# Kernel optimization log

Hardware: AMD Instinct MI355X
Metric: run time of the kernel (lower is better)

## Reference

```python
import jax, jax.numpy as jnp
import numpy as np

N = 50000   # nodes
E = 500000  # edges (before self-loops)
H = 4       # heads
C = 128     # per-head channels
DIN = 182
D1 = H * C  # 512
LN_EPS = 1e-5
NEG_SLOPE = 0.2


def setup_inputs():
    key = jax.random.key(0)
    ks = jax.random.split(key, 26)
    def rn(k, shape, s=0.05):
        return jax.random.normal(k, shape, jnp.float32) * s
    return {
        'x': jax.random.normal(ks[0], (N, DIN), jnp.float32),
        'edge_index': jax.random.randint(ks[1], (2, E), 0, N, jnp.int32),
        # GAT layer 1 (182 -> 4x128)
        'W1': rn(ks[2], (DIN, D1)), 'as1': rn(ks[3], (H, C)), 'ad1': rn(ks[4], (H, C)), 'b1': rn(ks[5], (D1,)),
        # LayerNorm 1
        'g1': jnp.ones((D1,), jnp.float32), 'bn1': jnp.zeros((D1,), jnp.float32),
        # Expansion MLP 512->512->256
        'We1': rn(ks[6], (D1, D1)), 'bE1': rn(ks[7], (D1,)),
        'We2': rn(ks[8], (D1, 256)), 'bE2': rn(ks[9], (256,)),
        # Residual projection 512->256 + learned scale
        'Wr': rn(ks[10], (D1, 256)), 'br': rn(ks[11], (256,)),
        'rscale': jnp.float32(0.5),
        # GAT layer 2 (256 -> 4x128)
        'W2': rn(ks[12], (256, D1)), 'as2': rn(ks[13], (H, C)), 'ad2': rn(ks[14], (H, C)), 'b2': rn(ks[15], (D1,)),
        # LayerNorm 2
        'g2': jnp.ones((D1,), jnp.float32), 'bn2': jnp.zeros((D1,), jnp.float32),
        # Classifier 512->512->2
        'Wc1': rn(ks[16], (D1, D1)), 'bc1': rn(ks[17], (D1,)),
        'Wc2': rn(ks[18], (D1, 2)), 'bc2': rn(ks[19], (2,)),
    }


def layer_norm(x, g, b):
    mu = jnp.mean(x, axis=-1, keepdims=True)
    var = jnp.mean(jnp.square(x - mu), axis=-1, keepdims=True)
    return (x - mu) * jax.lax.rsqrt(var + LN_EPS) * g + b


def gat_conv(x, src, dst, W, a_src, a_dst, bias):
    # PyG GATConv (eval mode, self-loops already in src/dst), concat heads.
    h = (x @ W).reshape(N, H, C)                     # [N,H,C]
    al_s = jnp.sum(h * a_src, axis=-1)               # [N,H]
    al_d = jnp.sum(h * a_dst, axis=-1)               # [N,H]
    e = jax.nn.leaky_relu(al_s[src] + al_d[dst], NEG_SLOPE)  # [E',H]
    m = jax.ops.segment_max(e, dst, num_segments=N)  # segment softmax over target nbhd
    ex = jnp.exp(e - m[dst])
    denom = jax.ops.segment_sum(ex, dst, num_segments=N)
    alpha = ex / denom[dst]                          # [E',H]
    msg = h[src] * alpha[:, :, None]                 # [E',H,C]
    out = jax.ops.segment_sum(msg, dst, num_segments=N)
    return out.reshape(N, H * C) + bias


def reference(x, edge_index, W1, as1, ad1, b1, g1, bn1, We1, bE1, We2, bE2,
              Wr, br, rscale, W2, as2, ad2, b2, g2, bn2, Wc1, bc1, Wc2, bc2):
    loops = jnp.arange(N, dtype=edge_index.dtype)
    src = jnp.concatenate([edge_index[0], loops])    # add self-loops (PyG default)
    dst = jnp.concatenate([edge_index[1], loops])

    h1 = gat_conv(x, src, dst, W1, as1, ad1, b1)
    h1 = jax.nn.elu(layer_norm(h1, g1, bn1))
    h_exp = jax.nn.relu(h1 @ We1 + bE1) @ We2 + bE2  # expansion MLP (dropout=eval)
    h_comb = (h1 @ Wr + br) + rscale * h_exp         # residual combine

    h2 = gat_conv(h_comb, src, dst, W2, as2, ad2, b2)
    h2 = jax.nn.elu(layer_norm(h2, g2, bn2))
    out = jax.nn.relu(h2 @ Wc1 + bc1) @ Wc2 + bc2    # classifier -> [N,2]
    return out
```

## Files before the change

kernel.cpp:

```cpp
#include <hip/hip_runtime.h>
#include <hip/hip_bf16.h>
#include <math.h>

#define NNODES 50000
#define NEDGES 500000
#define NTOT   (NEDGES + NNODES)
#define MPAD   50048
#define D1     512
#define NH     4
#define LN_EPS 1e-5f
#define NEG_SLOPE 0.2f

#define SBLK 256
#define NSB  ((NNODES + SBLK - 1) / SBLK)

typedef __attribute__((ext_vector_type(8))) short short8;
typedef __attribute__((ext_vector_type(4))) float f32x4;
typedef __hip_bfloat16 bf16;

#define GLDS16(g, l) __builtin_amdgcn_global_load_lds( \
    (const __attribute__((address_space(1))) void*)(g), \
    (__attribute__((address_space(3))) void*)(l), 16, 0, 0)

__device__ __forceinline__ float bf2f(short u) {
    unsigned int x = ((unsigned int)(unsigned short)u) << 16;
    return __uint_as_float(x);
}
__device__ __forceinline__ short f2bf(float f) {
    unsigned int x = __float_as_uint(f);
    unsigned int r = (x + 0x7fffu + ((x >> 16) & 1u)) >> 16;
    return (short)r;
}
__device__ __forceinline__ float leaky(float e) {
    return (e >= 0.f) ? e : NEG_SLOPE * e;
}


__global__ void k_count(const int* __restrict__ ei, int* __restrict__ counts) {
    int e = blockIdx.x * blockDim.x + threadIdx.x;
    if (e >= NTOT) return;
    int d = (e < NEDGES) ? ei[NEDGES + e] : (e - NEDGES);
    atomicAdd(&counts[d], 1);
}

__global__ void k_scan1(const int* __restrict__ counts, int* __restrict__ offs,
                        int* __restrict__ bsums) {
    __shared__ int s[SBLK];
    int tid = threadIdx.x, b = blockIdx.x;
    int idx = b * SBLK + tid;
    int v = (idx < NNODES) ? counts[idx] : 0;
    s[tid] = v;
    __syncthreads();
    for (int d = 1; d < SBLK; d <<= 1) {
        int t = (tid >= d) ? s[tid - d] : 0;
        __syncthreads();
        s[tid] += t;
        __syncthreads();
    }
    if (idx < NNODES) offs[idx] = s[tid] - v;
    if (tid == SBLK - 1) bsums[b] = s[tid];
}

__global__ void k_scan2(const int* __restrict__ bsums, int* __restrict__ bbase) {
    __shared__ int s[256];
    int tid = threadIdx.x;
    int v = (tid < NSB) ? bsums[tid] : 0;
    s[tid] = v;
    __syncthreads();
    for (int d = 1; d < 256; d <<= 1) {
        int t = (tid >= d) ? s[tid - d] : 0;
        __syncthreads();
        s[tid] += t;
        __syncthreads();
    }
    bbase[tid] = s[tid] - v;
    if (tid == 255) bbase[256] = s[255];
}

__global__ void k_scan3(int* __restrict__ offs, const int* __restrict__ bbase,
                        int* __restrict__ cursor) {
    int idx = blockIdx.x * 256 + threadIdx.x;
    if (idx < NNODES) {
        int v = offs[idx] + bbase[idx >> 8];
        offs[idx] = v;
        cursor[idx] = v;
    }
    if (idx == 0) offs[NNODES] = bbase[256];
}

__global__ void k_fill(const int* __restrict__ ei, int* __restrict__ cursor,
                       int* __restrict__ srcs) {
    int e = blockIdx.x * blockDim.x + threadIdx.x;
    if (e >= NTOT) return;
    int s, d;
    if (e < NEDGES) { s = ei[e]; d = ei[NEDGES + e]; }
    else            { s = d = e - NEDGES; }
    int pos = atomicAdd(&cursor[d], 1);
    srcs[pos] = s;
}


__global__ void k_wt_all(const float* __restrict__ W1, const float* __restrict__ We1,
                         const float* __restrict__ We2, const float* __restrict__ Wr,
                         const float* __restrict__ W2, const float* __restrict__ Wc1,
                         bf16* __restrict__ W1t, bf16* __restrict__ We1t,
                         bf16* __restrict__ We2t, bf16* __restrict__ Wrt,
                         bf16* __restrict__ W2t, bf16* __restrict__ Wc1t) {
    int which = blockIdx.y;
    const float* W; bf16* Wt; int K, N, Kpad;
    switch (which) {
        case 0:  W = W1;  Wt = W1t;  K = 182; N = 512; Kpad = 192; break;
        case 1:  W = We1; Wt = We1t; K = 512; N = 512; Kpad = 512; break;
        case 2:  W = We2; Wt = We2t; K = 512; N = 256; Kpad = 512; break;
        case 3:  W = Wr;  Wt = Wrt;  K = 512; N = 256; Kpad = 512; break;
        case 4:  W = W2;  Wt = W2t;  K = 256; N = 512; Kpad = 256; break;
        default: W = Wc1; Wt = Wc1t; K = 512; N = 512; Kpad = 512; break;
    }
    int idx = blockIdx.x * 256 + threadIdx.x;
    if (idx >= N * Kpad) return;
    int n = idx / Kpad, k = idx % Kpad;
    float v = (k < K) ? W[(size_t)k * N + n] : 0.f;
    Wt[idx] = __float2bfloat16(v);
}

__global__ void k_xconv(const float* __restrict__ x, bf16* __restrict__ xb) {
    int idx = blockIdx.x * 256 + threadIdx.x;
    if (idx >= MPAD * 192) return;
    int r = idx / 192, k = idx % 192;
    float v = (r < NNODES && k < 182) ? x[(size_t)r * 182 + k] : 0.f;
    xb[idx] = __float2bfloat16(v);
}


__global__ __launch_bounds__(256) void k_attn_logits(
        const bf16* __restrict__ h, const float* __restrict__ a_s,
        const float* __restrict__ a_d, float* __restrict__ als,
        float* __restrict__ ald) {
    int tid = threadIdx.x;
    int n = blockIdx.x * 4 + (tid >> 6);
    if (n >= NNODES) return;
    int lane = tid & 63;
    int ch0 = lane * 8;
    short8 hv = *reinterpret_cast<const short8*>(&h[(size_t)n * D1 + ch0]);
    float s1 = 0.f, s2 = 0.f;
    #pragma unroll
    for (int j = 0; j < 8; j++) {
        float v = bf2f(hv[j]);
        s1 += v * a_s[ch0 + j];
        s2 += v * a_d[ch0 + j];
    }
    #pragma unroll
    for (int o = 1; o < 16; o <<= 1) {
        s1 += __shfl_xor(s1, o);
        s2 += __shfl_xor(s2, o);
    }
    if ((lane & 15) == 0) {
        int head = lane >> 4;
        als[n * NH + head] = s1;
        ald[n * NH + head] = s2;
    }
}


__global__ __launch_bounds__(256) void k_edge_alpha(
        const float* __restrict__ als, const float* __restrict__ ald,
        const int* __restrict__ offs, const int* __restrict__ srcs,
        float* __restrict__ alpha) {
    int tid = threadIdx.x;
    int n = blockIdx.x * 4 + (tid >> 6);
    if (n >= NNODES) return;
    int lane = tid & 63;
    int head = lane >> 4, sub = lane & 15;
    int e0 = offs[n], e1 = offs[n + 1];
    float adh = ald[n * NH + head];

    float m = -1e30f;
    for (int k = e0 + sub; k < e1; k += 16)
        m = fmaxf(m, leaky(als[srcs[k] * NH + head] + adh));
    #pragma unroll
    for (int o = 1; o < 16; o <<= 1) m = fmaxf(m, __shfl_xor(m, o));
    float d = 0.f;
    for (int k = e0 + sub; k < e1; k += 16)
        d += __expf(leaky(als[srcs[k] * NH + head] + adh) - m);
    #pragma unroll
    for (int o = 1; o < 16; o <<= 1) d += __shfl_xor(d, o);
    float dinv = 1.f / d;
    for (int k = e0 + sub; k < e1; k += 16)
        alpha[k * NH + head] = __expf(leaky(als[srcs[k] * NH + head] + adh) - m) * dinv;
}


__global__ __launch_bounds__(256) void k_gat_aggregate(
        const bf16* __restrict__ h, const float* __restrict__ alpha,
        const int* __restrict__ offs, const int* __restrict__ srcs,
        const float* __restrict__ bias, const float* __restrict__ gamma,
        const float* __restrict__ beta, bf16* __restrict__ out) {
    int tid = threadIdx.x;
    int n = blockIdx.x * 4 + (tid >> 6);
    if (n >= NNODES) return;
    int lane = tid & 63;
    int head = lane >> 4;
    int ch0 = lane * 8;
    int e0 = offs[n], e1 = offs[n + 1];

    float acc[8] = {};
    for (int base = e0; base < e1; base += 64) {
        int cnt = min(64, e1 - base);
        int sv = (base + lane < e1) ? srcs[base + lane] : 0;
        int k = 0;
        for (; k + 4 <= cnt; k += 4) {
            int s0 = __shfl(sv, k),     s1 = __shfl(sv, k + 1);
            int s2 = __shfl(sv, k + 2), s3 = __shfl(sv, k + 3);
            float p0 = alpha[(base + k)     * NH + head];
            float p1 = alpha[(base + k + 1) * NH + head];
            float p2 = alpha[(base + k + 2) * NH + head];
            float p3 = alpha[(base + k + 3) * NH + head];
            short8 h0 = *reinterpret_cast<const short8*>(&h[(size_t)s0 * D1 + ch0]);
            short8 h1 = *reinterpret_cast<const short8*>(&h[(size_t)s1 * D1 + ch0]);
            short8 h2 = *reinterpret_cast<const short8*>(&h[(size_t)s2 * D1 + ch0]);
            short8 h3 = *reinterpret_cast<const short8*>(&h[(size_t)s3 * D1 + ch0]);
            #pragma unroll
            for (int j = 0; j < 8; j++)
                acc[j] += p0 * bf2f(h0[j]) + p1 * bf2f(h1[j])
                        + p2 * bf2f(h2[j]) + p3 * bf2f(h3[j]);
        }
        for (; k < cnt; k++) {
            int s0 = __shfl(sv, k);
            float p0 = alpha[(base + k) * NH + head];
            short8 h0 = *reinterpret_cast<const short8*>(&h[(size_t)s0 * D1 + ch0]);
            #pragma unroll
            for (int j = 0; j < 8; j++) acc[j] += p0 * bf2f(h0[j]);
        }
    }

    float v[8];
    float ps = 0.f;
    #pragma unroll
    for (int j = 0; j < 8; j++) { v[j] = acc[j] + bias[ch0 + j]; ps += v[j]; }
    #pragma unroll
    for (int o = 1; o < 64; o <<= 1) ps += __shfl_xor(ps, o);
    float mu = ps * (1.f / 512.f);
    float qs = 0.f;
    #pragma unroll
    for (int j = 0; j < 8; j++) { float dvj = v[j] - mu; qs += dvj * dvj; }
    #pragma unroll
    for (int o = 1; o < 64; o <<= 1) qs += __shfl_xor(qs, o);
    float rstd = rsqrtf(qs * (1.f / 512.f) + LN_EPS);

    short8 ov;
    #pragma unroll
    for (int j = 0; j < 8; j++) {
        float y = (v[j] - mu) * rstd * gamma[ch0 + j] + beta[ch0 + j];
        float e = (y > 0.f) ? y : (__expf(y) - 1.f);
        ov[j] = f2bf(e);
    }
    *reinterpret_cast<short8*>(&out[(size_t)n * D1 + ch0]) = ov;
}


#define EPI_BF       0
#define EPI_BRELU_BF 1
#define EPI_CLS      2

template<int EPI>
__global__ __launch_bounds__(256) void gemm_bf16(
    const ushort* __restrict__ A, const ushort* __restrict__ Bt,
    const float* __restrict__ bias, bf16* __restrict__ Obf,
    float* __restrict__ Of32, const float* __restrict__ Wc2,
    int Mreal, int N, int K, const float* __restrict__ bc2) {
    __shared__ __align__(16) ushort As[128 * 32];
    __shared__ __align__(16) ushort Bs[128 * 32];
    int tid = threadIdx.x;
    int wave = tid >> 6, lane = tid & 63;
    int brow = blockIdx.y * 128;
    int bcol = blockIdx.x * 128;
    int wm = (wave >> 1) * 64, wn = (wave & 1) * 64;

    f32x4 acc[4][4] = {};

    int ldr = lane >> 2;
    int ldk = (lane & 3) * 8;

    for (int k0 = 0; k0 < K; k0 += 32) {
        if (k0) __syncthreads();
        #pragma unroll
        for (int c2 = 0; c2 < 2; c2++) {
            int c = wave + c2 * 4;
            int row = c * 16 + ldr;
            GLDS16(A  + (size_t)(brow + row) * K + k0 + ldk, As + c * 512);
            GLDS16(Bt + (size_t)(bcol + row) * K + k0 + ldk, Bs + c * 512);
        }
        __syncthreads();

        short8 af[4], bfr[4];
        int lr = lane & 15, lk = (lane >> 4) * 8;
        #pragma unroll
        for (int f = 0; f < 4; f++) {
            af[f]  = *reinterpret_cast<const short8*>(&As[(wm + f * 16 + lr) * 32 + lk]);
            bfr[f] = *reinterpret_cast<const short8*>(&Bs[(wn + f * 16 + lr) * 32 + lk]);
        }
        #pragma unroll
        for (int fm = 0; fm < 4; fm++)
            #pragma unroll
            for (int fn = 0; fn < 4; fn++)
                acc[fm][fn] = __builtin_amdgcn_mfma_f32_16x16x32_bf16(
                    af[fm], bfr[fn], acc[fm][fn], 0, 0, 0);
    }

    if (EPI == EPI_CLS) {
        float w2[4][2], b4[4];
        #pragma unroll
        for (int fn = 0; fn < 4; fn++) {
            int col = bcol + wn + fn * 16 + (lane & 15);
            w2[fn][0] = Wc2[col * 2];
            w2[fn][1] = Wc2[col * 2 + 1];
            b4[fn] = bias[col];
        }
        #pragma unroll
        for (int fm = 0; fm < 4; fm++) {
            #pragma unroll
            for (int r = 0; r < 4; r++) {
                int row = brow + wm + fm * 16 + (lane >> 4) * 4 + r;
                float s0 = 0.f, s1 = 0.f;
                #pragma unroll
                for (int fn = 0; fn < 4; fn++) {
                    float v = acc[fm][fn][r] + b4[fn];
                    v = v > 0.f ? v : 0.f;
                    s0 += v * w2[fn][0];
                    s1 += v * w2[fn][1];
                }
                #pragma unroll
                for (int o = 1; o < 16; o <<= 1) {
                    s0 += __shfl_xor(s0, o);
                    s1 += __shfl_xor(s1, o);
                }
                if ((lane & 15) == 0 && row < Mreal) {
                    if (bcol == 0 && wn == 0) { s0 += bc2[0]; s1 += bc2[1]; }
                    atomicAdd(&Of32[row * 2],     s0);
                    atomicAdd(&Of32[row * 2 + 1], s1);
                }
            }
        }
        return;
    }

    #pragma unroll
    for (int fm = 0; fm < 4; fm++) {
        int row0 = brow + wm + fm * 16 + (lane >> 4) * 4;
        #pragma unroll
        for (int fn = 0; fn < 4; fn++) {
            int col = bcol + wn + fn * 16 + (lane & 15);
            #pragma unroll
            for (int r = 0; r < 4; r++) {
                int row = row0 + r;
                if (row >= Mreal) continue;
                size_t idx = (size_t)row * N + col;
                float v = acc[fm][fn][r];
                if (EPI == EPI_BF) {
                    Obf[idx] = __float2bfloat16(v);
                } else {
                    v += bias[col]; v = v > 0.f ? v : 0.f;
                    Obf[idx] = __float2bfloat16(v);
                }
            }
        }
    }
}


__global__ __launch_bounds__(256) void gemm_dual(
    const ushort* __restrict__ A1, const ushort* __restrict__ B1t,
    const ushort* __restrict__ A2, const ushort* __restrict__ B2t,
    const float* __restrict__ bias1, const float* __restrict__ bias2,
    bf16* __restrict__ Obf, int Mreal, int N, int K,
    const float* __restrict__ rsc) {
    __shared__ __align__(16) ushort As[128 * 32];
    __shared__ __align__(16) ushort Bs[128 * 32];
    int tid = threadIdx.x;
    int wave = tid >> 6, lane = tid & 63;
    int brow = blockIdx.y * 128;
    int bcol = blockIdx.x * 128;
    int wm = (wave >> 1) * 64, wn = (wave & 1) * 64;
    float rs = *rsc;

    f32x4 acc[4][4] = {};

    int ldr = lane >> 2;
    int ldk = (lane & 3) * 8;
    int lr = lane & 15, lk = (lane >> 4) * 8;

    #pragma unroll
    for (int phase = 0; phase < 2; phase++) {
        const ushort* Ap = phase ? A2 : A1;
        const ushort* Bp = phase ? B2t : B1t;
        if (phase) {
            __syncthreads();
            #pragma unroll
            for (int fm = 0; fm < 4; fm++)
                #pragma unroll
                for (int fn = 0; fn < 4; fn++)
                    #pragma unroll
                    for (int r = 0; r < 4; r++) acc[fm][fn][r] *= rs;
        }
        for (int k0 = 0; k0 < K; k0 += 32) {
            if (k0 || phase) __syncthreads();
            #pragma unroll
            for (int c2 = 0; c2 < 2; c2++) {
                int c = wave + c2 * 4;
                int row = c * 16 + ldr;
                GLDS16(Ap + (size_t)(brow + row) * K + k0 + ldk, As + c * 512);
                GLDS16(Bp + (size_t)(bcol + row) * K + k0 + ldk, Bs + c * 512);
            }
            __syncthreads();

            short8 af[4], bfr[4];
            #pragma unroll
            for (int f = 0; f < 4; f++) {
                af[f]  = *reinterpret_cast<const short8*>(&As[(wm + f * 16 + lr) * 32 + lk]);
                bfr[f] = *reinterpret_cast<const short8*>(&Bs[(wn + f * 16 + lr) * 32 + lk]);
            }
            #pragma unroll
            for (int fm = 0; fm < 4; fm++)
                #pragma unroll
                for (int fn = 0; fn < 4; fn++)
                    acc[fm][fn] = __builtin_amdgcn_mfma_f32_16x16x32_bf16(
                        af[fm], bfr[fn], acc[fm][fn], 0, 0, 0);
        }
    }

    #pragma unroll
    for (int fm = 0; fm < 4; fm++) {
        int row0 = brow + wm + fm * 16 + (lane >> 4) * 4;
        #pragma unroll
        for (int fn = 0; fn < 4; fn++) {
            int col = bcol + wn + fn * 16 + (lane & 15);
            float be = bias2[col] + rs * bias1[col];
            #pragma unroll
            for (int r = 0; r < 4; r++) {
                int row = row0 + r;
                if (row >= Mreal) continue;
                Obf[(size_t)row * N + col] = __float2bfloat16(acc[fm][fn][r] + be);
            }
        }
    }
}


extern "C" void kernel_launch(void* const* d_in, const int* in_sizes, int n_in,
                              void* d_out, int out_size, void* d_ws, size_t ws_size,
                              hipStream_t stream) {
    const float* x   = (const float*)d_in[0];
    const int*   ei  = (const int*)d_in[1];
    const float* W1  = (const float*)d_in[2];
    const float* as1 = (const float*)d_in[3];
    const float* ad1 = (const float*)d_in[4];
    const float* b1  = (const float*)d_in[5];
    const float* g1  = (const float*)d_in[6];
    const float* bn1 = (const float*)d_in[7];
    const float* We1 = (const float*)d_in[8];
    const float* bE1 = (const float*)d_in[9];
    const float* We2 = (const float*)d_in[10];
    const float* bE2 = (const float*)d_in[11];
    const float* Wr  = (const float*)d_in[12];
    const float* br  = (const float*)d_in[13];
    const float* rsc = (const float*)d_in[14];
    const float* W2  = (const float*)d_in[15];
    const float* as2 = (const float*)d_in[16];
    const float* ad2 = (const float*)d_in[17];
    const float* b2  = (const float*)d_in[18];
    const float* g2  = (const float*)d_in[19];
    const float* bn2 = (const float*)d_in[20];
    const float* Wc1 = (const float*)d_in[21];
    const float* bc1 = (const float*)d_in[22];
    const float* Wc2 = (const float*)d_in[23];
    const float* bc2 = (const float*)d_in[24];
    float* out = (float*)d_out;

    char* ws = (char*)d_ws;
    size_t o = 0;
    auto alloc = [&](size_t bytes) { void* p = ws + o; o += (bytes + 255) & ~255ull; return p; };
    bf16* xb    = (bf16*)alloc((size_t)MPAD * 192 * 2);
    bf16* bufA  = (bf16*)alloc((size_t)MPAD * D1 * 2);
    bf16* bufB  = (bf16*)alloc((size_t)MPAD * D1 * 2);
    bf16* bufC  = (bf16*)alloc((size_t)MPAD * D1 * 2);
    bf16* hcb   = (bf16*)alloc((size_t)MPAD * 256 * 2);
    bf16* W1t   = (bf16*)alloc((size_t)512 * 192 * 2);
    bf16* We1t  = (bf16*)alloc((size_t)512 * 512 * 2);
    bf16* We2t  = (bf16*)alloc((size_t)256 * 512 * 2);
    bf16* Wrt   = (bf16*)alloc((size_t)256 * 512 * 2);
    bf16* W2t   = (bf16*)alloc((size_t)512 * 256 * 2);
    bf16* Wc1t  = (bf16*)alloc((size_t)512 * 512 * 2);
    float* als  = (float*)alloc((size_t)NNODES * NH * 4);
    float* ald  = (float*)alloc((size_t)NNODES * NH * 4);
    float* alpha= (float*)alloc((size_t)NTOT * NH * 4);
    int* counts = (int*)alloc((NNODES + 1) * 4);
    int* offs   = (int*)alloc((NNODES + 1) * 4);
    int* cursor = (int*)alloc((NNODES + 1) * 4);
    int* srcs   = (int*)alloc((size_t)NTOT * 4);
    int* bsums  = (int*)alloc((NSB + 1) * 4);
    int* bbase  = (int*)alloc(257 * 4);

    hipMemsetAsync(counts, 0, NNODES * 4, stream);
    k_count<<<(NTOT + 255) / 256, 256, 0, stream>>>(ei, counts);
    k_scan1<<<NSB, SBLK, 0, stream>>>(counts, offs, bsums);
    k_scan2<<<1, 256, 0, stream>>>(bsums, bbase);
    k_scan3<<<(NNODES + 255) / 256, 256, 0, stream>>>(offs, bbase, cursor);
    k_fill<<<(NTOT + 255) / 256, 256, 0, stream>>>(ei, cursor, srcs);

    k_wt_all<<<dim3(1024, 6), 256, 0, stream>>>(W1, We1, We2, Wr, W2, Wc1,
                                                W1t, We1t, We2t, Wrt, W2t, Wc1t);
    k_xconv<<<(MPAD * 192 + 255) / 256, 256, 0, stream>>>(x, xb);

    dim3 blk(256);
    dim3 g512(4, MPAD / 128), g256(2, MPAD / 128);
    int nwb = (NNODES + 3) / 4;

    gemm_bf16<EPI_BF><<<g512, blk, 0, stream>>>((const ushort*)xb, (const ushort*)W1t,
        nullptr, bufA, nullptr, nullptr, NNODES, 512, 192, nullptr);
    k_attn_logits<<<nwb, blk, 0, stream>>>(bufA, as1, ad1, als, ald);
    k_edge_alpha<<<nwb, blk, 0, stream>>>(als, ald, offs, srcs, alpha);
    k_gat_aggregate<<<nwb, blk, 0, stream>>>(bufA, alpha, offs, srcs, b1, g1, bn1, bufB);

    gemm_bf16<EPI_BRELU_BF><<<g512, blk, 0, stream>>>((const ushort*)bufB, (const ushort*)We1t,
        bE1, bufC, nullptr, nullptr, NNODES, 512, 512, nullptr);
    gemm_dual<<<g256, blk, 0, stream>>>((const ushort*)bufC, (const ushort*)We2t,
        (const ushort*)bufB, (const ushort*)Wrt, bE2, br, hcb, NNODES, 256, 512, rsc);

    gemm_bf16<EPI_BF><<<g512, blk, 0, stream>>>((const ushort*)hcb, (const ushort*)W2t,
        nullptr, bufA, nullptr, nullptr, NNODES, 512, 256, nullptr);
    k_attn_logits<<<nwb, blk, 0, stream>>>(bufA, as2, ad2, als, ald);
    k_edge_alpha<<<nwb, blk, 0, stream>>>(als, ald, offs, srcs, alpha);
    k_gat_aggregate<<<nwb, blk, 0, stream>>>(bufA, alpha, offs, srcs, b2, g2, bn2, bufB);

    hipMemsetAsync(out, 0, (size_t)out_size * 4, stream);
    gemm_bf16<EPI_CLS><<<g512, blk, 0, stream>>>((const ushort*)bufB, (const ushort*)Wc1t,
        bc1, nullptr, out, Wc2, NNODES, 512, 512, bc2);
}
```

Measured before the change: 561.0 us.

## Use K=64 swizzled LDS tiles, fuse attention logits into GEMM epilogue, reorder grid

```diff
diff --git a/kernel.cpp b/kernel.cpp
--- a/kernel.cpp
+++ b/kernel.cpp
@@ -129,36 +129,6 @@
     int r = idx / 192, k = idx % 192;
     float v = (r < NNODES && k < 182) ? x[(size_t)r * 182 + k] : 0.f;
     xb[idx] = __float2bfloat16(v);
-}
-
-
-__global__ __launch_bounds__(256) void k_attn_logits(
-        const bf16* __restrict__ h, const float* __restrict__ a_s,
-        const float* __restrict__ a_d, float* __restrict__ als,
-        float* __restrict__ ald) {
-    int tid = threadIdx.x;
-    int n = blockIdx.x * 4 + (tid >> 6);
-    if (n >= NNODES) return;
-    int lane = tid & 63;
-    int ch0 = lane * 8;
-    short8 hv = *reinterpret_cast<const short8*>(&h[(size_t)n * D1 + ch0]);
-    float s1 = 0.f, s2 = 0.f;
-    #pragma unroll
-    for (int j = 0; j < 8; j++) {
-        float v = bf2f(hv[j]);
-        s1 += v * a_s[ch0 + j];
-        s2 += v * a_d[ch0 + j];
-    }
-    #pragma unroll
-    for (int o = 1; o < 16; o <<= 1) {
-        s1 += __shfl_xor(s1, o);
-        s2 += __shfl_xor(s2, o);
-    }
-    if ((lane & 15) == 0) {
-        int head = lane >> 4;
-        als[n * NH + head] = s1;
-        ald[n * NH + head] = s2;
-    }
 }
 
 
@@ -258,60 +228,102 @@
 }
 
 
-#define EPI_BF       0
+#define EPI_BF_LOG   0
 #define EPI_BRELU_BF 1
 #define EPI_CLS      2
 
 template<int EPI>
-__global__ __launch_bounds__(256) void gemm_bf16(
+__global__ __launch_bounds__(256) void gemm64(
     const ushort* __restrict__ A, const ushort* __restrict__ Bt,
     const float* __restrict__ bias, bf16* __restrict__ Obf,
     float* __restrict__ Of32, const float* __restrict__ Wc2,
-    int Mreal, int N, int K, const float* __restrict__ bc2) {
-    __shared__ __align__(16) ushort As[128 * 32];
-    __shared__ __align__(16) ushort Bs[128 * 32];
+    int Mreal, int N, int K, const float* __restrict__ bc2,
+    const float* __restrict__ a_s, const float* __restrict__ a_d,
+    float* __restrict__ als, float* __restrict__ ald) {
+    __shared__ __align__(16) ushort As[128 * 64];
+    __shared__ __align__(16) ushort Bs[128 * 64];
     int tid = threadIdx.x;
     int wave = tid >> 6, lane = tid & 63;
-    int brow = blockIdx.y * 128;
-    int bcol = blockIdx.x * 128;
+    int brow = blockIdx.x * 128;
+    int bcol = blockIdx.y * 128;
     int wm = (wave >> 1) * 64, wn = (wave & 1) * 64;
+    int lr = lane & 15, hi = lane >> 4;
+    int rx = lr & 7;
+    int r8 = lane >> 3;
+    int slotsw = (lane & 7) ^ r8;
 
     f32x4 acc[4][4] = {};
 
-    int ldr = lane >> 2;
-    int ldk = (lane & 3) * 8;
-
-    for (int k0 = 0; k0 < K; k0 += 32) {
+    for (int k0 = 0; k0 < K; k0 += 64) {
         if (k0) __syncthreads();
         #pragma unroll
-        for (int c2 = 0; c2 < 2; c2++) {
-            int c = wave + c2 * 4;
-            int row = c * 16 + ldr;
-            GLDS16(A  + (size_t)(brow + row) * K + k0 + ldk, As + c * 512);
-            GLDS16(Bt + (size_t)(bcol + row) * K + k0 + ldk, Bs + c * 512);
+        for (int i = 0; i < 4; i++) {
+            int rb = wave * 32 + i * 8;
+            GLDS16(A  + (size_t)(brow + rb + r8) * K + k0 + slotsw * 8, As + rb * 64);
+            GLDS16(Bt + (size_t)(bcol + rb + r8) * K + k0 + slotsw * 8, Bs + rb * 64);
         }
         __syncthreads();
 
-        short8 af[4], bfr[4];
-        int lr = lane & 15, lk = (lane >> 4) * 8;
-        #pragma unroll
-        for (int f = 0; f < 4; f++) {
-            af[f]  = *reinterpret_cast<const short8*>(&As[(wm + f * 16 + lr) * 32 + lk]);
-            bfr[f] = *reinterpret_cast<const short8*>(&Bs[(wn + f * 16 + lr) * 32 + lk]);
-        }
-        #pragma unroll
-        for (int fm = 0; fm < 4; fm++)
-            #pragma unroll
-            for (int fn = 0; fn < 4; fn++)
-                acc[fm][fn] = __builtin_amdgcn_mfma_f32_16x16x32_bf16(
-                    af[fm], bfr[fn], acc[fm][fn], 0, 0, 0);
+        #pragma unroll
+        for (int sub = 0; sub < 2; sub++) {
+            short8 af[4], bfr[4];
+            int bsl = ((sub * 4 + hi) ^ rx) * 8;
+            #pragma unroll
+            for (int f = 0; f < 4; f++) {
+                af[f]  = *reinterpret_cast<const short8*>(&As[(wm + f * 16 + lr) * 64 + bsl]);
+                bfr[f] = *reinterpret_cast<const short8*>(&Bs[(wn + f * 16 + lr) * 64 + bsl]);
+            }
+            #pragma unroll
+            for (int fm = 0; fm < 4; fm++)
+                #pragma unroll
+                for (int fn = 0; fn < 4; fn++)
+                    acc[fm][fn] = __builtin_amdgcn_mfma_f32_16x16x32_bf16(
+                        af[fm], bfr[fn], acc[fm][fn], 0, 0, 0);
+        }
+    }
+
+    if (EPI == EPI_BF_LOG) {
+        int head = bcol >> 7;
+        float asr[4], adr[4];
+        #pragma unroll
+        for (int fn = 0; fn < 4; fn++) {
+            int col = bcol + wn + fn * 16 + lr;
+            asr[fn] = a_s[col]; adr[fn] = a_d[col];
+        }
+        #pragma unroll
+        for (int fm = 0; fm < 4; fm++) {
+            int row0 = brow + wm + fm * 16 + hi * 4;
+            #pragma unroll
+            for (int r = 0; r < 4; r++) {
+                int row = row0 + r;
+                bool ok = row < Mreal;
+                float s1 = 0.f, s2 = 0.f;
+                #pragma unroll
+                for (int fn = 0; fn < 4; fn++) {
+                    float v = acc[fm][fn][r];
+                    if (ok) Obf[(size_t)row * N + bcol + wn + fn * 16 + lr] = __float2bfloat16(v);
+                    s1 += v * asr[fn];
+                    s2 += v * adr[fn];
+                }
+                #pragma unroll
+                for (int o = 1; o < 16; o <<= 1) {
+                    s1 += __shfl_xor(s1, o);
+                    s2 += __shfl_xor(s2, o);
+                }
+                if (ok && lr == 0) {
+                    atomicAdd(&als[row * NH + head], s1);
+                    atomicAdd(&ald[row * NH + head], s2);
+                }
+            }
+        }
+        return;
     }
 
     if (EPI == EPI_CLS) {
         float w2[4][2], b4[4];
         #pragma unroll
         for (int fn = 0; fn < 4; fn++) {
-            int col = bcol + wn + fn * 16 + (lane & 15);
+            int col = bcol + wn + fn * 16 + lr;
             w2[fn][0] = Wc2[col * 2];
             w2[fn][1] = Wc2[col * 2 + 1];
             b4[fn] = bias[col];
@@ -320,7 +332,7 @@
         for (int fm = 0; fm < 4; fm++) {
             #pragma unroll
             for (int r = 0; r < 4; r++) {
-                int row = brow + wm + fm * 16 + (lane >> 4) * 4 + r;
+                int row = brow + wm + fm * 16 + hi * 4 + r;
                 float s0 = 0.f, s1 = 0.f;
                 #pragma unroll
                 for (int fn = 0; fn < 4; fn++) {
@@ -334,7 +346,7 @@
                     s0 += __shfl_xor(s0, o);
                     s1 += __shfl_xor(s1, o);
                 }
-                if ((lane & 15) == 0 && row < Mreal) {
+                if (lr == 0 && row < Mreal) {
                     if (bcol == 0 && wn == 0) { s0 += bc2[0]; s1 += bc2[1]; }
                     atomicAdd(&Of32[row * 2],     s0);
                     atomicAdd(&Of32[row * 2 + 1], s1);
@@ -346,48 +358,43 @@
 
     #pragma unroll
     for (int fm = 0; fm < 4; fm++) {
-        int row0 = brow + wm + fm * 16 + (lane >> 4) * 4;
+        int row0 = brow + wm + fm * 16 + hi * 4;
         #pragma unroll
         for (int fn = 0; fn < 4; fn++) {
-            int col = bcol + wn + fn * 16 + (lane & 15);
+            int col = bcol + wn + fn * 16 + lr;
             #pragma unroll
             for (int r = 0; r < 4; r++) {
                 int row = row0 + r;
                 if (row >= Mreal) continue;
-                size_t idx = (size_t)row * N + col;
-                float v = acc[fm][fn][r];
-                if (EPI == EPI_BF) {
-                    Obf[idx] = __float2bfloat16(v);
-                } else {
-                    v += bias[col]; v = v > 0.f ? v : 0.f;
-                    Obf[idx] = __float2bfloat16(v);
-                }
-            }
-        }
-    }
-}
-
-
-__global__ __launch_bounds__(256) void gemm_dual(
+                float v = acc[fm][fn][r] + bias[col];
+                v = v > 0.f ? v : 0.f;
+                Obf[(size_t)row * N + col] = __float2bfloat16(v);
+            }
+        }
+    }
+}
+
+
+__global__ __launch_bounds__(256) void gemm_dual64(
     const ushort* __restrict__ A1, const ushort* __restrict__ B1t,
     const ushort* __restrict__ A2, const ushort* __restrict__ B2t,
     const float* __restrict__ bias1, const float* __restrict__ bias2,
     bf16* __restrict__ Obf, int Mreal, int N, int K,
     const float* __restrict__ rsc) {
-    __shared__ __align__(16) ushort As[128 * 32];
-    __shared__ __align__(16) ushort Bs[128 * 32];
+    __shared__ __align__(16) ushort As[128 * 64];
+    __shared__ __align__(16) ushort Bs[128 * 64];
     int tid = threadIdx.x;
     int wave = tid >> 6, lane = tid & 63;
-    int brow = blockIdx.y * 128;
-    int bcol = blockIdx.x * 128;
+    int brow = blockIdx.x * 128;
+    int bcol = blockIdx.y * 128;
     int wm = (wave >> 1) * 64, wn = (wave & 1) * 64;
+    int lr = lane & 15, hi = lane >> 4;
+    int rx = lr & 7;
+    int r8 = lane >> 3;
+    int slotsw = (lane & 7) ^ r8;
     float rs = *rsc;
 
     f32x4 acc[4][4] = {};
-
-    int ldr = lane >> 2;
-    int ldk = (lane & 3) * 8;
-    int lr = lane & 15, lk = (lane >> 4) * 8;
 
     #pragma unroll
     for (int phase = 0; phase < 2; phase++) {
@@ -402,38 +409,41 @@
                     #pragma unroll
                     for (int r = 0; r < 4; r++) acc[fm][fn][r] *= rs;
         }
-        for (int k0 = 0; k0 < K; k0 += 32) {
+        for (int k0 = 0; k0 < K; k0 += 64) {
             if (k0 || phase) __syncthreads();
             #pragma unroll
-            for (int c2 = 0; c2 < 2; c2++) {
-                int c = wave + c2 * 4;
-                int row = c * 16 + ldr;
-                GLDS16(Ap + (size_t)(brow + row) * K + k0 + ldk, As + c * 512);
-                GLDS16(Bp + (size_t)(bcol + row) * K + k0 + ldk, Bs + c * 512);
+            for (int i = 0; i < 4; i++) {
+                int rb = wave * 32 + i * 8;
+                GLDS16(Ap + (size_t)(brow + rb + r8) * K + k0 + slotsw * 8, As + rb * 64);
+                GLDS16(Bp + (size_t)(bcol + rb + r8) * K + k0 + slotsw * 8, Bs + rb * 64);
             }
             __syncthreads();
 
-            short8 af[4], bfr[4];
-            #pragma unroll
-            for (int f = 0; f < 4; f++) {
-                af[f]  = *reinterpret_cast<const short8*>(&As[(wm + f * 16 + lr) * 32 + lk]);
-                bfr[f] = *reinterpret_cast<const short8*>(&Bs[(wn + f * 16 + lr) * 32 + lk]);
-            }
-            #pragma unroll
-            for (int fm = 0; fm < 4; fm++)
-                #pragma unroll
-                for (int fn = 0; fn < 4; fn++)
-                    acc[fm][fn] = __builtin_amdgcn_mfma_f32_16x16x32_bf16(
-                        af[fm], bfr[fn], acc[fm][fn], 0, 0, 0);
+            #pragma unroll
+            for (int sub = 0; sub < 2; sub++) {
+                short8 af[4], bfr[4];
+                int bsl = ((sub * 4 + hi) ^ rx) * 8;
+                #pragma unroll
+                for (int f = 0; f < 4; f++) {
+                    af[f]  = *reinterpret_cast<const short8*>(&As[(wm + f * 16 + lr) * 64 + bsl]);
+                    bfr[f] = *reinterpret_cast<const short8*>(&Bs[(wn + f * 16 + lr) * 64 + bsl]);
+                }
+                #pragma unroll
+                for (int fm = 0; fm < 4; fm++)
+                    #pragma unroll
+                    for (int fn = 0; fn < 4; fn++)
+                        acc[fm][fn] = __builtin_amdgcn_mfma_f32_16x16x32_bf16(
+                            af[fm], bfr[fn], acc[fm][fn], 0, 0, 0);
+            }
         }
     }
 
     #pragma unroll
     for (int fm = 0; fm < 4; fm++) {
-        int row0 = brow + wm + fm * 16 + (lane >> 4) * 4;
+        int row0 = brow + wm + fm * 16 + hi * 4;
         #pragma unroll
         for (int fn = 0; fn < 4; fn++) {
-            int col = bcol + wn + fn * 16 + (lane & 15);
+            int col = bcol + wn + fn * 16 + lr;
             float be = bias2[col] + rs * bias1[col];
             #pragma unroll
             for (int r = 0; r < 4; r++) {
@@ -512,27 +522,27 @@
     k_xconv<<<(MPAD * 192 + 255) / 256, 256, 0, stream>>>(x, xb);
 
     dim3 blk(256);
-    dim3 g512(4, MPAD / 128), g256(2, MPAD / 128);
+    dim3 g512(MPAD / 128, 4), g256(MPAD / 128, 2);
     int nwb = (NNODES + 3) / 4;
 
-    gemm_bf16<EPI_BF><<<g512, blk, 0, stream>>>((const ushort*)xb, (const ushort*)W1t,
-        nullptr, bufA, nullptr, nullptr, NNODES, 512, 192, nullptr);
-    k_attn_logits<<<nwb, blk, 0, stream>>>(bufA, as1, ad1, als, ald);
+    hipMemsetAsync(als, 0, (size_t)NNODES * NH * 4 * 2, stream);
+    gemm64<EPI_BF_LOG><<<g512, blk, 0, stream>>>((const ushort*)xb, (const ushort*)W1t,
+        nullptr, bufA, nullptr, nullptr, NNODES, 512, 192, nullptr, as1, ad1, als, ald);
     k_edge_alpha<<<nwb, blk, 0, stream>>>(als, ald, offs, srcs, alpha);
     k_gat_aggregate<<<nwb, blk, 0, stream>>>(bufA, alpha, offs, srcs, b1, g1, bn1, bufB);
 
-    gemm_bf16<EPI_BRELU_BF><<<g512, blk, 0, stream>>>((const ushort*)bufB, (const ushort*)We1t,
-        bE1, bufC, nullptr, nullptr, NNODES, 512, 512, nullptr);
-    gemm_dual<<<g256, blk, 0, stream>>>((const ushort*)bufC, (const ushort*)We2t,
+    gemm64<EPI_BRELU_BF><<<g512, blk, 0, stream>>>((const ushort*)bufB, (const ushort*)We1t,
+        bE1, bufC, nullptr, nullptr, NNODES, 512, 512, nullptr, nullptr, nullptr, nullptr, nullptr);
+    gemm_dual64<<<g256, blk, 0, stream>>>((const ushort*)bufC, (const ushort*)We2t,
         (const ushort*)bufB, (const ushort*)Wrt, bE2, br, hcb, NNODES, 256, 512, rsc);
 
-    gemm_bf16<EPI_BF><<<g512, blk, 0, stream>>>((const ushort*)hcb, (const ushort*)W2t,
-        nullptr, bufA, nullptr, nullptr, NNODES, 512, 256, nullptr);
-    k_attn_logits<<<nwb, blk, 0, stream>>>(bufA, as2, ad2, als, ald);
+    hipMemsetAsync(als, 0, (size_t)NNODES * NH * 4 * 2, stream);
+    gemm64<EPI_BF_LOG><<<g512, blk, 0, stream>>>((const ushort*)hcb, (const ushort*)W2t,
+        nullptr, bufA, nullptr, nullptr, NNODES, 512, 256, nullptr, as2, ad2, als, ald);
     k_edge_alpha<<<nwb, blk, 0, stream>>>(als, ald, offs, srcs, alpha);
     k_gat_aggregate<<<nwb, blk, 0, stream>>>(bufA, alpha, offs, srcs, b2, g2, bn2, bufB);
 
     hipMemsetAsync(out, 0, (size_t)out_size * 4, stream);
-    gemm_bf16<EPI_CLS><<<g512, blk, 0, stream>>>((const ushort*)bufB, (const ushort*)Wc1t,
-        bc1, nullptr, out, Wc2, NNODES, 512, 512, bc2);
-}
+    gemm64<EPI_CLS><<<g512, blk, 0, stream>>>((const ushort*)bufB, (const ushort*)Wc1t,
+        bc1, nullptr, out, Wc2, NNODES, 512, 512, bc2, nullptr, nullptr, nullptr, nullptr);
+}
```

Result: slower. 585.2 us (+4.3%).
